# Kernel tuning notes

Measured on AMD Instinct MI355X. Metric: run time of the kernel, lower is better.

Reference implementation:

```python
import jax, jax.numpy as jnp
import numpy as np

BANDS = [2,3,3,3,3,3,3,3,3,3,3,8,8,8,8,8,8,8,8,8,8,8,8,16,16,16,16,16,16,16,17]
C = 128      # channels
H = 512      # 4 * channels
MAXO = 17 * 12  # padded fc2 output dim (largest band)
EPS = 1e-5


def setup_inputs() -> dict:
    key = jax.random.key(0)
    k0, k1, k2, k3, k4 = jax.random.split(key, 5)
    B, T, K = 4, 2000, len(BANDS)
    x = jax.random.normal(k0, (B, C, T, K), jnp.float32)
    norm_w = jnp.ones((K, C), jnp.float32)
    norm_b = jnp.zeros((K, C), jnp.float32)
    fc1_w = jax.random.normal(k1, (K, H, C), jnp.float32) * 0.05
    fc1_b = jax.random.normal(k2, (K, H), jnp.float32) * 0.02
    fc2_w = jax.random.normal(k3, (K, MAXO, H), jnp.float32) * 0.05
    fc2_b = jax.random.normal(k4, (K, MAXO), jnp.float32) * 0.02
    return dict(x=x, norm_w=norm_w, norm_b=norm_b, fc1_w=fc1_w, fc1_b=fc1_b,
                fc2_w=fc2_w, fc2_b=fc2_b)


def reference(x, norm_w, norm_b, fc1_w, fc1_b, fc2_w, fc2_b):
    # x: [B, C, T, K]. GroupNorm(1, C) per band: normalize over (C, T), affine per channel.
    mean = jnp.mean(x, axis=(1, 2), keepdims=True)            # [B,1,1,K]
    var = jnp.var(x, axis=(1, 2), keepdims=True)
    xn = (x - mean) / jnp.sqrt(var + EPS)
    xn = xn * norm_w.T[None, :, None, :] + norm_b.T[None, :, None, :]
    # fc1 + tanh, batched over all bands (same shape per band, distinct weights)
    h = jnp.einsum('bctk,khc->btkh', xn, fc1_w) + fc1_b       # [B,T,K,H]
    h = jnp.tanh(h)
    # fc2 + GLU per band (heterogeneous output dims -> small fixed loop)
    outs = []
    for i, bw in enumerate(BANDS):
        o = h[:, :, i, :] @ fc2_w[i, :12 * bw].T + fc2_b[i, :12 * bw]  # [B,T,12*bw]
        a, g = jnp.split(o, 2, axis=-1)
        o = a * jax.nn.sigmoid(g)                             # GLU -> [B,T,6*bw]
        outs.append(o.reshape(o.shape[0], o.shape[1], bw, 3, 2))
    m = jnp.concatenate(outs, axis=2)                         # [B,T,257,3,2]
    return m.transpose(0, 2, 1, 3, 4)                         # [B,257,T,3,2]
```

## Files before the change

### kernel.cpp

```cpp
#include <hip/hip_runtime.h>
#include <hip/hip_bf16.h>

#define NBANDS 31
#define CDIM 128
#define TDIM 2000
#define HDIM 512
#define MTOT 8000
#define MAXO 204
#define OPAD 224
#define NGRP 124
#define NMTILE 504
#define NMBK 63

typedef __attribute__((ext_vector_type(8))) short short8;
typedef __attribute__((ext_vector_type(4))) float f32x4;
typedef __attribute__((ext_vector_type(4))) unsigned int u32x4;
typedef __bf16 bf16x8 __attribute__((ext_vector_type(8)));

__constant__ int d_bw[NBANDS]   = {2,3,3,3,3,3,3,3,3,3,3,8,8,8,8,8,8,8,8,8,8,8,8,16,16,16,16,16,16,16,17};
__constant__ int d_boff[NBANDS] = {0,2,5,8,11,14,17,20,23,26,29,32,40,48,56,64,72,80,88,96,104,112,120,128,144,160,176,192,208,224,240};
__constant__ int d_nn16[NBANDS] = {2,3,3,3,3,3,3,3,3,3,3,6,6,6,6,6,6,6,6,6,6,6,6,12,12,12,12,12,12,12,13};

__device__ __forceinline__ unsigned short f2bf(float f) {
  unsigned int u = __float_as_uint(f);
  return (unsigned short)((u + 0x7fffu + ((u >> 16) & 1u)) >> 16);
}

__device__ __forceinline__ unsigned int cvt_pk_bf16(float lo, float hi) {
  unsigned int r;
  asm("v_cvt_pk_bf16_f32 %0, %1, %2" : "=v"(r) : "v"(lo), "v"(hi));
  return r;
}

__device__ __forceinline__ float fast_tanh(float x) {
  float p = __builtin_amdgcn_exp2f(2.885390082f * x);
  return 1.0f - 2.0f * __builtin_amdgcn_rcpf(p + 1.0f);
}

__device__ __forceinline__ float fast_sigmoid(float x) {
  return __builtin_amdgcn_rcpf(1.0f + __builtin_amdgcn_exp2f(-1.442695041f * x));
}

__device__ __forceinline__ f32x4 mfma_bf16(short8 a, short8 b, f32x4 c) {
  return __builtin_amdgcn_mfma_f32_16x16x32_bf16(
      __builtin_bit_cast(bf16x8, a), __builtin_bit_cast(bf16x8, b), c, 0, 0, 0);
}

__device__ __forceinline__ void g2lds(const char* gsrc, char* ldst, int lane) {
  __builtin_amdgcn_global_load_lds(
      (const __attribute__((address_space(1))) unsigned int*)(gsrc + lane * 16),
      (__attribute__((address_space(3))) unsigned int*)ldst, 16, 0, 0);
}

__global__ void k_finalize(const float* __restrict__ wsum, const float* __restrict__ wsq,
                           float* __restrict__ gmean, float* __restrict__ grstd) {
  int g = threadIdx.x;
  if (g < NGRP) {
    const float n = (float)(CDIM * TDIM);
    float m = wsum[g] / n;
    float v = wsq[g] / n - m * m;
    gmean[g] = m;
    grstd[g] = rsqrtf(v + 1e-5f);
  }
}

__global__ void k_prep_w1(const float* __restrict__ fc1_w, const float* __restrict__ norm_w,
                          const float* __restrict__ norm_b, const float* __restrict__ fc1_b,
                          unsigned short* __restrict__ w1f, float* __restrict__ t1,
                          float* __restrict__ t2) {
  int kn = blockIdx.x;
  int k = kn >> 9, n = kn & 511;
  int c = threadIdx.x;
  float w  = fc1_w[(size_t)kn * CDIM + c];
  float nw = norm_w[k * CDIM + c];
  float nb = norm_b[k * CDIM + c];
  float wp = w * nw;
  {
    int nc = n >> 7, hh = (n >> 4) & 7, kk = c >> 5;
    int lnw = (n & 15) | (((c >> 3) & 3) << 4);
    size_t eoff = ((((size_t)(k * 4 + nc) * 8 + hh) * 4 + kk) * 64 + lnw) * 8 + (c & 7);
    w1f[eoff] = f2bf(wp);
  }
  float s1 = wp, s2 = w * nb;
  #pragma unroll
  for (int off = 32; off >= 1; off >>= 1) {
    s1 += __shfl_down(s1, off);
    s2 += __shfl_down(s2, off);
  }
  __shared__ float r1[2], r2[2];
  if ((threadIdx.x & 63) == 0) { r1[threadIdx.x >> 6] = s1; r2[threadIdx.x >> 6] = s2; }
  __syncthreads();
  if (threadIdx.x == 0) {
    t1[kn] = r1[0] + r1[1];
    t2[kn] = r2[0] + r2[1] + fc1_b[kn];
  }
}

__global__ void k_prep_w2(const float* __restrict__ fc2_w, const float* __restrict__ fc2_b,
                          unsigned short* __restrict__ w2f, float* __restrict__ b2) {
  int ko = blockIdx.x;
  int k = ko >> 8;
  int o = ko & 255;
  int bw = d_bw[k];
  int O2 = 12 * bw, hf = 6 * bw;
  bool valid = o < O2;
  int srcrow = valid ? ((o & 1) ? (hf + (o >> 1)) : (o >> 1)) : 0;
  const float* sp = fc2_w + ((size_t)k * MAXO + srcrow) * HDIM;
  if (threadIdx.x == 0 && o < OPAD)
    b2[k * OPAD + o] = valid ? fc2_b[k * MAXO + srcrow] : 0.f;
  int ot = o >> 4, rr = o & 15;
  for (int j = threadIdx.x; j < HDIM; j += 256) {
    int ks = j >> 5, hp = j & 31;
    int q  = (hp >> 2) & 3;
    int jj = ((hp >> 4) << 2) | (hp & 3);
    unsigned short val = valid ? f2bf(sp[j]) : (unsigned short)0;
    size_t eoff = (((size_t)(k * 16 + ks)) * 16 + ot) * 512 + (size_t)(rr | (q << 4)) * 8 + jj;
    w2f[eoff] = val;
  }
}

__global__ void k_transpose(const float* __restrict__ x, unsigned short* __restrict__ xtf,
                            float* __restrict__ wsum, float* __restrict__ wsq) {
  __shared__ unsigned short tile[248 * 128];
  __shared__ float sred[256], sqred[256];
  const int t0 = blockIdx.x * 8;
  const int b = blockIdx.y;
  const int tid = threadIdx.x;
  const float* p = x + ((size_t)b * CDIM * TDIM + t0) * NBANDS;
  float s = 0.f, sq = 0.f;
  if (tid < 248) {
    const int f = tid;
    char* row = (char*)tile + f * 256;
    const int st = 4 * f;
    #pragma unroll 4
    for (int c2 = 0; c2 < 64; ++c2) {
      float v0 = p[(size_t)c2 * 124000 + f];
      float v1 = p[(size_t)c2 * 124000 + 62000 + f];
      s += v0 + v1;
      sq += v0 * v0 + v1 * v1;
      *(unsigned int*)(row + ((4 * c2 + st) & 255)) = cvt_pk_bf16(v0, v1);
    }
  }
  sred[tid] = s; sqred[tid] = sq;
  __syncthreads();
  if (tid < 31) {
    float ss = 0.f, qs = 0.f;
    #pragma unroll
    for (int j = 0; j < 8; ++j) { ss += sred[tid + 31 * j]; qs += sqred[tid + 31 * j]; }
    atomicAdd(&wsum[b * 31 + tid], ss);
    atomicAdd(&wsq [b * 31 + tid], qs);
  }
  for (int idx = tid; idx < 3968; idx += 256) {
    int ti = idx & 7, q4w = (idx >> 3) & 3, kkw = (idx >> 5) & 3, kb = idx >> 7;
    int f = ti * 31 + kb;
    const char* row = (const char*)tile + f * 256;
    const int st = 4 * f;
    u32x4 v;
    #pragma unroll
    for (int j = 0; j < 4; ++j)
      v[j] = *(const unsigned int*)(row + ((kkw * 64 + q4w * 16 + 4 * j + st) & 255));
    int m = b * TDIM + t0 + ti;
    int mtile = m >> 4, mrow = m & 15;
    size_t eoff = ((((size_t)kb * NMTILE + mtile) * 4 + kkw) * 64 + (mrow | (q4w << 4))) * 8;
    *(u32x4*)(xtf + eoff) = v;
  }
}

template<int SMAX>
__launch_bounds__(256, 2)
__global__ void k_gemm(const unsigned short* __restrict__ xtf,
                       const unsigned short* __restrict__ w1f,
                       const float* __restrict__ t1p, const float* __restrict__ t2p,
                       const unsigned short* __restrict__ w2f,
                       const float* __restrict__ b2p,
                       const float* __restrict__ gmean, const float* __restrict__ grstd,
                       float* __restrict__ out, int kbase, int nwg) {
  extern __shared__ char lds[];
  constexpr int BUFB = (8 + SMAX) * 1024;
  float* const t12 = (float*)lds;
  char* const bufA = lds + 4096;
  char* const bufB = lds + 4096 + BUFB;
  float* const Ls  = (float*)lds;

  const int bid = blockIdx.x;
  const int qq = nwg >> 3, r8 = nwg & 7;
  const int xcd = bid & 7, ixd = bid >> 3;
  const int wg = (xcd < r8 ? xcd * (qq + 1) : r8 * (qq + 1) + (xcd - r8) * qq) + ixd;
  const int kl = wg / NMBK;
  const int k = kbase + kl;
  const int mb = wg - kl * NMBK;
  const int m0 = mb * 128;

  const int tid = threadIdx.x;
  const int lane = tid & 63;
  const int wid = tid >> 6;
  const int col = lane & 15;
  const int q4 = lane >> 4;

  const int bw = d_bw[k];
  const int nn = d_nn16[k];
  const int half = 6 * bw;
  const int boffk = d_boff[k];

  #pragma unroll
  for (int i = 0; i < 2; ++i) {
    t12[tid + i * 256] = t1p[k * HDIM + tid + i * 256];
    t12[512 + tid + i * 256] = t2p[k * HDIM + tid + i * 256];
  }

  const int mt0 = (m0 >> 4) + wid * 2;
  short8 xv[2][4];
  #pragma unroll
  for (int r = 0; r < 2; ++r)
    #pragma unroll
    for (int kk = 0; kk < 4; ++kk)
      xv[r][kk] = *(const short8*)(xtf +
          (((size_t)k * NMTILE + mt0 + r) * 4 + kk) * 512 + lane * 8);

  float rs[2], rm[2];
  #pragma unroll
  for (int r = 0; r < 2; ++r) {
    int mr = m0 + wid * 32 + r * 16 + col;
    int mc = mr < (MTOT - 1) ? mr : (MTOT - 1);
    int g = (mc / 2000) * NBANDS + k;
    rs[r] = grstd[g];
    rm[r] = rs[r] * gmean[g];
  }

  const char* const w1kc = (const char*)w1f + (size_t)k * 131072;
  const char* const w2kc = (const char*)w2f + (size_t)k * 262144;
  const int ntt = 8 + nn;

  auto stage = [&](char* buf, int c) {
    const char* w1c = w1kc + (((c >> 2) * 8 + (c & 3) * 2) * 4096);
    const char* w2c = w2kc + c * 16384;
    for (int t = wid; t < ntt; t += 4) {
      const char* src = (t < 8) ? (w1c + t * 1024) : (w2c + (t - 8) * 1024);
      g2lds(src, buf + t * 1024, lane);
    }
  };

  const f32x4 fz = {0.f, 0.f, 0.f, 0.f};
  f32x4 acc2[SMAX][2];
  #pragma unroll
  for (int s = 0; s < SMAX; ++s) { acc2[s][0] = fz; acc2[s][1] = fz; }

  stage(bufA, 0);
  __syncthreads();

  #pragma unroll 1
  for (int c = 0; c < 16; ++c) {
    char* const bc = (c & 1) ? bufB : bufA;
    if (c < 15) stage((c & 1) ? bufA : bufB, c + 1);

    f32x4 a1[2][2];
    a1[0][0] = fz; a1[0][1] = fz; a1[1][0] = fz; a1[1][1] = fz;
    #pragma unroll
    for (int kk = 0; kk < 4; ++kk) {
      short8 wa0 = *(const short8*)(bc + kk * 1024 + lane * 16);
      short8 wa1 = *(const short8*)(bc + 4096 + kk * 1024 + lane * 16);
      #pragma unroll
      for (int r = 0; r < 2; ++r) {
        a1[0][r] = mfma_bf16(wa0, xv[r][kk], a1[0][r]);
        a1[1][r] = mfma_bf16(wa1, xv[r][kk], a1[1][r]);
      }
    }
    short8 hb[2];
    #pragma unroll
    for (int r = 0; r < 2; ++r) {
      u32x4 hbw;
      #pragma unroll
      for (int ht = 0; ht < 2; ++ht) {
        const f32x4 c1 = *(const f32x4*)(t12 + c * 32 + ht * 16 + q4 * 4);
        const f32x4 c2 = *(const f32x4*)(t12 + 512 + c * 32 + ht * 16 + q4 * 4);
        f32x4 v = a1[ht][r];
        float e0 = fast_tanh(fmaf(rs[r], v[0], fmaf(-rm[r], c1[0], c2[0])));
        float e1 = fast_tanh(fmaf(rs[r], v[1], fmaf(-rm[r], c1[1], c2[1])));
        float e2 = fast_tanh(fmaf(rs[r], v[2], fmaf(-rm[r], c1[2], c2[2])));
        float e3 = fast_tanh(fmaf(rs[r], v[3], fmaf(-rm[r], c1[3], c2[3])));
        hbw[ht * 2]     = cvt_pk_bf16(e0, e1);
        hbw[ht * 2 + 1] = cvt_pk_bf16(e2, e3);
      }
      hb[r] = __builtin_bit_cast(short8, hbw);
    }
    const char* w2l = bc + 8192;
    #pragma unroll
    for (int s = 0; s < SMAX; ++s) {
      if (s < nn) {
        short8 wb = *(const short8*)(w2l + s * 1024 + lane * 16);
        acc2[s][0] = mfma_bf16(wb, hb[0], acc2[s][0]);
        acc2[s][1] = mfma_bf16(wb, hb[1], acc2[s][1]);
      }
    }
    __syncthreads();
  }

  const float* b2k = b2p + (size_t)k * OPAD;
  const bool plain = (m0 / 2000 == (m0 + 127) / 2000) && (m0 + 128 <= MTOT);
  if (plain) {
    #pragma unroll
    for (int s = 0; s < SMAX; ++s) {
      if (s < nn) {
        f32x4 bias = *(const f32x4*)(b2k + s * 16 + q4 * 4);
        #pragma unroll
        for (int r = 0; r < 2; ++r) {
          const int tloc = wid * 32 + r * 16 + col;
          f32x4 v = acc2[s][r];
          #pragma unroll
          for (int p = 0; p < 2; ++p) {
            float a = v[2 * p] + bias[2 * p];
            float g = v[2 * p + 1] + bias[2 * p + 1];
            int op = s * 8 + q4 * 2 + p;
            if (op < half) {
              int orr = op / 6, occ = op - orr * 6;
              Ls[(orr * 128 + tloc) * 6 + occ] = a * fast_sigmoid(g);
            }
          }
        }
      }
    }
    __syncthreads();
    const int bb = m0 / 2000;
    const int tb = m0 - bb * 2000;
    const size_t obase = ((size_t)bb * 257 + boffk) * 2000;
    const int tot = bw * 384;
    for (int ii = tid; ii < tot; ii += 256) {
      int orr = ii / 384;
      int rem = ii - orr * 384;
      *(unsigned long long*)(out + (obase + (size_t)orr * 2000 + tb) * 6 + rem * 2) =
          *(const unsigned long long*)(Ls + orr * 768 + rem * 2);
    }
  } else {
    #pragma unroll
    for (int s = 0; s < SMAX; ++s) {
      if (s < nn) {
        f32x4 bias = *(const f32x4*)(b2k + s * 16 + q4 * 4);
        #pragma unroll
        for (int r = 0; r < 2; ++r) {
          const int m = m0 + wid * 32 + r * 16 + col;
          f32x4 v = acc2[s][r];
          #pragma unroll
          for (int p = 0; p < 2; ++p) {
            float a = v[2 * p] + bias[2 * p];
            float g = v[2 * p + 1] + bias[2 * p + 1];
            int op = s * 8 + q4 * 2 + p;
            if (op < half && m < MTOT) {
              int bbm = m / 2000;
              int t = m - bbm * 2000;
              int orr = op / 6, occ = op - orr * 6;
              out[(((size_t)bbm * 257 + boffk + orr) * TDIM + t) * 6 + occ] =
                  a * fast_sigmoid(g);
            }
          }
        }
      }
    }
  }
}

extern "C" void kernel_launch(void* const* d_in, const int* in_sizes, int n_in,
                              void* d_out, int out_size, void* d_ws, size_t ws_size,
                              hipStream_t stream) {
  const float* x      = (const float*)d_in[0];
  const float* norm_w = (const float*)d_in[1];
  const float* norm_b = (const float*)d_in[2];
  const float* fc1_w  = (const float*)d_in[3];
  const float* fc1_b  = (const float*)d_in[4];
  const float* fc2_w  = (const float*)d_in[5];
  const float* fc2_b  = (const float*)d_in[6];
  float* out = (float*)d_out;
  char* ws = (char*)d_ws;

  float* wsum  = (float*)(ws);
  float* wsq   = (float*)(ws + 512);
  float* gmean = (float*)(ws + 1024);
  float* grstd = (float*)(ws + 1536);
  size_t off = 4096;
  unsigned short* xtf = (unsigned short*)(ws + off); off += (size_t)NBANDS * NMTILE * 4 * 512 * 2;
  unsigned short* w1f = (unsigned short*)(ws + off); off += (size_t)NBANDS * 4 * 8 * 4 * 512 * 2;
  float* t1p = (float*)(ws + off); off += (size_t)NBANDS * HDIM * 4;
  float* t2p = (float*)(ws + off); off += (size_t)NBANDS * HDIM * 4;
  unsigned short* w2f = (unsigned short*)(ws + off); off += (size_t)NBANDS * 16 * 16 * 512 * 2;
  float* b2p = (float*)(ws + off); off += (size_t)NBANDS * OPAD * 4;

  hipMemsetAsync(ws, 0, 1024, stream);
  hipLaunchKernelGGL(k_prep_w1, dim3(NBANDS * HDIM), dim3(128), 0, stream,
                     fc1_w, norm_w, norm_b, fc1_b, w1f, t1p, t2p);
  hipLaunchKernelGGL(k_prep_w2, dim3(NBANDS * 256), dim3(256), 0, stream,
                     fc2_w, fc2_b, w2f, b2p);
  hipLaunchKernelGGL(k_transpose, dim3(250, 4), dim3(256), 0, stream, x, xtf, wsum, wsq);
  hipLaunchKernelGGL(k_finalize, dim3(1), dim3(128), 0, stream, wsum, wsq, gmean, grstd);

  hipFuncSetAttribute((const void*)k_gemm<13>, hipFuncAttributeMaxDynamicSharedMemorySize, 52224);
  hipFuncSetAttribute((const void*)k_gemm<6>,  hipFuncAttributeMaxDynamicSharedMemorySize, 32768);
  hipFuncSetAttribute((const void*)k_gemm<3>,  hipFuncAttributeMaxDynamicSharedMemorySize, 26624);
  hipLaunchKernelGGL((k_gemm<13>), dim3(8 * NMBK),  dim3(256), 52224, stream,
                     xtf, w1f, t1p, t2p, w2f, b2p, gmean, grstd, out, 23, 8 * NMBK);
  hipLaunchKernelGGL((k_gemm<6>),  dim3(12 * NMBK), dim3(256), 32768, stream,
                     xtf, w1f, t1p, t2p, w2f, b2p, gmean, grstd, out, 11, 12 * NMBK);
  hipLaunchKernelGGL((k_gemm<3>),  dim3(11 * NMBK), dim3(256), 26624, stream,
                     xtf, w1f, t1p, t2p, w2f, b2p, gmean, grstd, out, 0,  11 * NMBK);
}
```

Before: 194.9 us.

## Fuse preprocessing kernels and merge per-band GEMM launches into one

```diff
diff --git a/kernel.cpp b/kernel.cpp
--- a/kernel.cpp
+++ b/kernel.cpp
@@ -8,9 +8,10 @@
 #define MTOT 8000
 #define MAXO 204
 #define OPAD 224
-#define NGRP 124
 #define NMTILE 504
 #define NMBK 63
+#define NWGU (NBANDS * NMBK)
+#define SMAX 13
 
 typedef __attribute__((ext_vector_type(8))) short short8;
 typedef __attribute__((ext_vector_type(4))) float f32x4;
@@ -52,143 +53,143 @@
       (__attribute__((address_space(3))) unsigned int*)ldst, 16, 0, 0);
 }
 
-__global__ void k_finalize(const float* __restrict__ wsum, const float* __restrict__ wsq,
-                           float* __restrict__ gmean, float* __restrict__ grstd) {
-  int g = threadIdx.x;
-  if (g < NGRP) {
-    const float n = (float)(CDIM * TDIM);
-    float m = wsum[g] / n;
-    float v = wsq[g] / n - m * m;
-    gmean[g] = m;
-    grstd[g] = rsqrtf(v + 1e-5f);
-  }
-}
-
-__global__ void k_prep_w1(const float* __restrict__ fc1_w, const float* __restrict__ norm_w,
-                          const float* __restrict__ norm_b, const float* __restrict__ fc1_b,
-                          unsigned short* __restrict__ w1f, float* __restrict__ t1,
-                          float* __restrict__ t2) {
-  int kn = blockIdx.x;
-  int k = kn >> 9, n = kn & 511;
-  int c = threadIdx.x;
-  float w  = fc1_w[(size_t)kn * CDIM + c];
-  float nw = norm_w[k * CDIM + c];
-  float nb = norm_b[k * CDIM + c];
-  float wp = w * nw;
-  {
-    int nc = n >> 7, hh = (n >> 4) & 7, kk = c >> 5;
-    int lnw = (n & 15) | (((c >> 3) & 3) << 4);
-    size_t eoff = ((((size_t)(k * 4 + nc) * 8 + hh) * 4 + kk) * 64 + lnw) * 8 + (c & 7);
-    w1f[eoff] = f2bf(wp);
-  }
-  float s1 = wp, s2 = w * nb;
-  #pragma unroll
-  for (int off = 32; off >= 1; off >>= 1) {
-    s1 += __shfl_down(s1, off);
-    s2 += __shfl_down(s2, off);
-  }
-  __shared__ float r1[2], r2[2];
-  if ((threadIdx.x & 63) == 0) { r1[threadIdx.x >> 6] = s1; r2[threadIdx.x >> 6] = s2; }
-  __syncthreads();
-  if (threadIdx.x == 0) {
-    t1[kn] = r1[0] + r1[1];
-    t2[kn] = r2[0] + r2[1] + fc1_b[kn];
-  }
-}
-
-__global__ void k_prep_w2(const float* __restrict__ fc2_w, const float* __restrict__ fc2_b,
-                          unsigned short* __restrict__ w2f, float* __restrict__ b2) {
-  int ko = blockIdx.x;
-  int k = ko >> 8;
-  int o = ko & 255;
-  int bw = d_bw[k];
-  int O2 = 12 * bw, hf = 6 * bw;
-  bool valid = o < O2;
-  int srcrow = valid ? ((o & 1) ? (hf + (o >> 1)) : (o >> 1)) : 0;
-  const float* sp = fc2_w + ((size_t)k * MAXO + srcrow) * HDIM;
-  if (threadIdx.x == 0 && o < OPAD)
-    b2[k * OPAD + o] = valid ? fc2_b[k * MAXO + srcrow] : 0.f;
-  int ot = o >> 4, rr = o & 15;
-  for (int j = threadIdx.x; j < HDIM; j += 256) {
-    int ks = j >> 5, hp = j & 31;
-    int q  = (hp >> 2) & 3;
-    int jj = ((hp >> 4) << 2) | (hp & 3);
-    unsigned short val = valid ? f2bf(sp[j]) : (unsigned short)0;
-    size_t eoff = (((size_t)(k * 16 + ks)) * 16 + ot) * 512 + (size_t)(rr | (q << 4)) * 8 + jj;
-    w2f[eoff] = val;
-  }
-}
-
-__global__ void k_transpose(const float* __restrict__ x, unsigned short* __restrict__ xtf,
-                            float* __restrict__ wsum, float* __restrict__ wsq) {
+__launch_bounds__(256)
+__global__ void k_pre(const float* __restrict__ x,
+                      const float* __restrict__ norm_w, const float* __restrict__ norm_b,
+                      const float* __restrict__ fc1_w, const float* __restrict__ fc1_b,
+                      const float* __restrict__ fc2_w, const float* __restrict__ fc2_b,
+                      unsigned short* __restrict__ xtf,
+                      float* __restrict__ wsumP, float* __restrict__ wsqP,
+                      unsigned short* __restrict__ w1f,
+                      float* __restrict__ t1, float* __restrict__ t2,
+                      unsigned short* __restrict__ w2f, float* __restrict__ b2) {
   __shared__ unsigned short tile[248 * 128];
   __shared__ float sred[256], sqred[256];
-  const int t0 = blockIdx.x * 8;
-  const int b = blockIdx.y;
+  const int bid = blockIdx.x;
   const int tid = threadIdx.x;
-  const float* p = x + ((size_t)b * CDIM * TDIM + t0) * NBANDS;
-  float s = 0.f, sq = 0.f;
-  if (tid < 248) {
-    const int f = tid;
-    char* row = (char*)tile + f * 256;
-    const int st = 4 * f;
-    #pragma unroll 4
-    for (int c2 = 0; c2 < 64; ++c2) {
-      float v0 = p[(size_t)c2 * 124000 + f];
-      float v1 = p[(size_t)c2 * 124000 + 62000 + f];
-      s += v0 + v1;
-      sq += v0 * v0 + v1 * v1;
-      *(unsigned int*)(row + ((4 * c2 + st) & 255)) = cvt_pk_bf16(v0, v1);
-    }
-  }
-  sred[tid] = s; sqred[tid] = sq;
-  __syncthreads();
-  if (tid < 31) {
-    float ss = 0.f, qs = 0.f;
-    #pragma unroll
-    for (int j = 0; j < 8; ++j) { ss += sred[tid + 31 * j]; qs += sqred[tid + 31 * j]; }
-    atomicAdd(&wsum[b * 31 + tid], ss);
-    atomicAdd(&wsq [b * 31 + tid], qs);
-  }
-  for (int idx = tid; idx < 3968; idx += 256) {
-    int ti = idx & 7, q4w = (idx >> 3) & 3, kkw = (idx >> 5) & 3, kb = idx >> 7;
-    int f = ti * 31 + kb;
-    const char* row = (const char*)tile + f * 256;
-    const int st = 4 * f;
-    u32x4 v;
-    #pragma unroll
-    for (int j = 0; j < 4; ++j)
-      v[j] = *(const unsigned int*)(row + ((kkw * 64 + q4w * 16 + 4 * j + st) & 255));
-    int m = b * TDIM + t0 + ti;
-    int mtile = m >> 4, mrow = m & 15;
-    size_t eoff = ((((size_t)kb * NMTILE + mtile) * 4 + kkw) * 64 + (mrow | (q4w << 4))) * 8;
-    *(u32x4*)(xtf + eoff) = v;
-  }
-}
-
-template<int SMAX>
+
+  if (bid < 1000) {
+    const int tc = bid % 250, b = bid / 250;
+    const int t0 = tc * 8;
+    const float* p = x + ((size_t)b * CDIM * TDIM + t0) * NBANDS;
+    float s = 0.f, sq = 0.f;
+    if (tid < 248) {
+      const int f = tid;
+      char* row = (char*)tile + f * 256;
+      const int st = 4 * f;
+      #pragma unroll 4
+      for (int c2 = 0; c2 < 64; ++c2) {
+        float v0 = p[(size_t)c2 * 124000 + f];
+        float v1 = p[(size_t)c2 * 124000 + 62000 + f];
+        s += v0 + v1;
+        sq += v0 * v0 + v1 * v1;
+        *(unsigned int*)(row + ((4 * c2 + st) & 255)) = cvt_pk_bf16(v0, v1);
+      }
+    }
+    sred[tid] = s; sqred[tid] = sq;
+    __syncthreads();
+    if (tid < 31) {
+      float ss = 0.f, qs = 0.f;
+      #pragma unroll
+      for (int j = 0; j < 8; ++j) { ss += sred[tid + 31 * j]; qs += sqred[tid + 31 * j]; }
+      wsumP[((size_t)b * 250 + tc) * 31 + tid] = ss;
+      wsqP [((size_t)b * 250 + tc) * 31 + tid] = qs;
+    }
+    for (int idx = tid; idx < 3968; idx += 256) {
+      int ti = idx & 7, q4w = (idx >> 3) & 3, kkw = (idx >> 5) & 3, kb = idx >> 7;
+      int f = ti * 31 + kb;
+      const char* row = (const char*)tile + f * 256;
+      const int st = 4 * f;
+      u32x4 v;
+      #pragma unroll
+      for (int j = 0; j < 4; ++j)
+        v[j] = *(const unsigned int*)(row + ((kkw * 64 + q4w * 16 + 4 * j + st) & 255));
+      int m = b * TDIM + t0 + ti;
+      int mtile = m >> 4, mrow = m & 15;
+      size_t eoff = ((((size_t)kb * NMTILE + mtile) * 4 + kkw) * 64 + (mrow | (q4w << 4))) * 8;
+      *(u32x4*)(xtf + eoff) = v;
+    }
+  } else if (bid < 1992) {
+    const int idx = bid - 1000;
+    const int c = tid & 127;
+    const int hf2 = tid >> 7;
+    #pragma unroll 1
+    for (int it = 0; it < 8; ++it) {
+      const int kn = idx * 16 + it * 2 + hf2;
+      const int k = kn >> 9, n = kn & 511;
+      float w  = fc1_w[(size_t)kn * CDIM + c];
+      float nw = norm_w[k * CDIM + c];
+      float nb = norm_b[k * CDIM + c];
+      float wp = w * nw;
+      {
+        int nc = n >> 7, hh = (n >> 4) & 7, kk = c >> 5;
+        int lnw = (n & 15) | (((c >> 3) & 3) << 4);
+        size_t eoff = ((((size_t)(k * 4 + nc) * 8 + hh) * 4 + kk) * 64 + lnw) * 8 + (c & 7);
+        w1f[eoff] = f2bf(wp);
+      }
+      float s1 = wp, s2 = w * nb;
+      #pragma unroll
+      for (int off = 32; off >= 1; off >>= 1) {
+        s1 += __shfl_down(s1, off);
+        s2 += __shfl_down(s2, off);
+      }
+      if ((tid & 63) == 0) { sred[tid >> 6] = s1; sqred[tid >> 6] = s2; }
+      __syncthreads();
+      if ((tid & 127) == 0) {
+        t1[kn] = sred[hf2 * 2] + sred[hf2 * 2 + 1];
+        t2[kn] = sqred[hf2 * 2] + sqred[hf2 * 2 + 1] + fc1_b[kn];
+      }
+      __syncthreads();
+    }
+  } else {
+    const int idx = bid - 1992;
+    #pragma unroll 1
+    for (int oi = 0; oi < 8; ++oi) {
+      const int ko = idx * 8 + oi;
+      const int k = ko >> 8;
+      const int o = ko & 255;
+      const int bw = d_bw[k];
+      const int O2 = 12 * bw, hf = 6 * bw;
+      const bool valid = o < O2;
+      const int srcrow = valid ? ((o & 1) ? (hf + (o >> 1)) : (o >> 1)) : 0;
+      const float* sp = fc2_w + ((size_t)k * MAXO + srcrow) * HDIM;
+      if (tid == 0 && o < OPAD)
+        b2[k * OPAD + o] = valid ? fc2_b[k * MAXO + srcrow] : 0.f;
+      const int ot = o >> 4, rr = o & 15;
+      for (int j = tid; j < HDIM; j += 256) {
+        int ks = j >> 5, hp = j & 31;
+        int q  = (hp >> 2) & 3;
+        int jj = ((hp >> 4) << 2) | (hp & 3);
+        unsigned short val = valid ? f2bf(sp[j]) : (unsigned short)0;
+        size_t eoff = (((size_t)(k * 16 + ks)) * 16 + ot) * 512 + (size_t)(rr | (q << 4)) * 8 + jj;
+        w2f[eoff] = val;
+      }
+    }
+  }
+}
+
 __launch_bounds__(256, 2)
 __global__ void k_gemm(const unsigned short* __restrict__ xtf,
                        const unsigned short* __restrict__ w1f,
                        const float* __restrict__ t1p, const float* __restrict__ t2p,
                        const unsigned short* __restrict__ w2f,
                        const float* __restrict__ b2p,
-                       const float* __restrict__ gmean, const float* __restrict__ grstd,
-                       float* __restrict__ out, int kbase, int nwg) {
+                       const float* __restrict__ wsumP, const float* __restrict__ wsqP,
+                       float* __restrict__ out) {
   extern __shared__ char lds[];
   constexpr int BUFB = (8 + SMAX) * 1024;
   float* const t12 = (float*)lds;
   char* const bufA = lds + 4096;
   char* const bufB = lds + 4096 + BUFB;
+  float* const sstat = (float*)(lds + 4096 + 2 * BUFB);
   float* const Ls  = (float*)lds;
 
   const int bid = blockIdx.x;
-  const int qq = nwg >> 3, r8 = nwg & 7;
+  const int qq = NWGU >> 3, r8 = NWGU & 7;
   const int xcd = bid & 7, ixd = bid >> 3;
   const int wg = (xcd < r8 ? xcd * (qq + 1) : r8 * (qq + 1) + (xcd - r8) * qq) + ixd;
-  const int kl = wg / NMBK;
-  const int k = kbase + kl;
-  const int mb = wg - kl * NMBK;
+  const int k = wg / NMBK;
+  const int mb = wg - k * NMBK;
   const int m0 = mb * 128;
 
   const int tid = threadIdx.x;
@@ -202,29 +203,33 @@
   const int half = 6 * bw;
   const int boffk = d_boff[k];
 
+  const int b0 = m0 / 2000;
+  const int b1 = ((m0 + 127 < MTOT) ? (m0 + 127) : (MTOT - 1)) / 2000;
+  if (wid <= b1 - b0) {
+    const int b = b0 + wid;
+    float sP = 0.f, sQ = 0.f;
+    for (int t = lane; t < 250; t += 64) {
+      sP += wsumP[((size_t)b * 250 + t) * 31 + k];
+      sQ += wsqP [((size_t)b * 250 + t) * 31 + k];
+    }
+    #pragma unroll
+    for (int off = 32; off >= 1; off >>= 1) {
+      sP += __shfl_down(sP, off);
+      sQ += __shfl_down(sQ, off);
+    }
+    if (lane == 0) {
+      const float n = (float)(CDIM * TDIM);
+      float mean = sP / n;
+      float var = sQ / n - mean * mean;
+      sstat[wid * 2] = mean;
+      sstat[wid * 2 + 1] = rsqrtf(var + 1e-5f);
+    }
+  }
+
   #pragma unroll
   for (int i = 0; i < 2; ++i) {
     t12[tid + i * 256] = t1p[k * HDIM + tid + i * 256];
     t12[512 + tid + i * 256] = t2p[k * HDIM + tid + i * 256];
-  }
-
-  const int mt0 = (m0 >> 4) + wid * 2;
-  short8 xv[2][4];
-  #pragma unroll
-  for (int r = 0; r < 2; ++r)
-    #pragma unroll
-    for (int kk = 0; kk < 4; ++kk)
-      xv[r][kk] = *(const short8*)(xtf +
-          (((size_t)k * NMTILE + mt0 + r) * 4 + kk) * 512 + lane * 8);
-
-  float rs[2], rm[2];
-  #pragma unroll
-  for (int r = 0; r < 2; ++r) {
-    int mr = m0 + wid * 32 + r * 16 + col;
-    int mc = mr < (MTOT - 1) ? mr : (MTOT - 1);
-    int g = (mc / 2000) * NBANDS + k;
-    rs[r] = grstd[g];
-    rm[r] = rs[r] * gmean[g];
   }
 
   const char* const w1kc = (const char*)w1f + (size_t)k * 131072;
@@ -239,14 +244,33 @@
       g2lds(src, buf + t * 1024, lane);
     }
   };
+  stage(bufA, 0);
+
+  const int mt0 = (m0 >> 4) + wid * 2;
+  short8 xv[2][4];
+  #pragma unroll
+  for (int r = 0; r < 2; ++r)
+    #pragma unroll
+    for (int kk = 0; kk < 4; ++kk)
+      xv[r][kk] = *(const short8*)(xtf +
+          (((size_t)k * NMTILE + mt0 + r) * 4 + kk) * 512 + lane * 8);
+
+  __syncthreads();
+
+  float rs[2], rm[2];
+  #pragma unroll
+  for (int r = 0; r < 2; ++r) {
+    int mr = m0 + wid * 32 + r * 16 + col;
+    int mc = mr < (MTOT - 1) ? mr : (MTOT - 1);
+    int bsel = mc / 2000 - b0;
+    rs[r] = sstat[bsel * 2 + 1];
+    rm[r] = rs[r] * sstat[bsel * 2];
+  }
 
   const f32x4 fz = {0.f, 0.f, 0.f, 0.f};
   f32x4 acc2[SMAX][2];
   #pragma unroll
   for (int s = 0; s < SMAX; ++s) { acc2[s][0] = fz; acc2[s][1] = fz; }
-
-  stage(bufA, 0);
-  __syncthreads();
 
   #pragma unroll 1
   for (int c = 0; c < 16; ++c) {
@@ -371,11 +395,9 @@
   float* out = (float*)d_out;
   char* ws = (char*)d_ws;
 
-  float* wsum  = (float*)(ws);
-  float* wsq   = (float*)(ws + 512);
-  float* gmean = (float*)(ws + 1024);
-  float* grstd = (float*)(ws + 1536);
-  size_t off = 4096;
+  size_t off = 0;
+  float* wsumP = (float*)(ws + off); off += (size_t)4 * 250 * 31 * 4 + 128;
+  float* wsqP  = (float*)(ws + off); off += (size_t)4 * 250 * 31 * 4 + 128;
   unsigned short* xtf = (unsigned short*)(ws + off); off += (size_t)NBANDS * NMTILE * 4 * 512 * 2;
   unsigned short* w1f = (unsigned short*)(ws + off); off += (size_t)NBANDS * 4 * 8 * 4 * 512 * 2;
   float* t1p = (float*)(ws + off); off += (size_t)NBANDS * HDIM * 4;
@@ -383,21 +405,11 @@
   unsigned short* w2f = (unsigned short*)(ws + off); off += (size_t)NBANDS * 16 * 16 * 512 * 2;
   float* b2p = (float*)(ws + off); off += (size_t)NBANDS * OPAD * 4;
 
-  hipMemsetAsync(ws, 0, 1024, stream);
-  hipLaunchKernelGGL(k_prep_w1, dim3(NBANDS * HDIM), dim3(128), 0, stream,
-                     fc1_w, norm_w, norm_b, fc1_b, w1f, t1p, t2p);
-  hipLaunchKernelGGL(k_prep_w2, dim3(NBANDS * 256), dim3(256), 0, stream,
-                     fc2_w, fc2_b, w2f, b2p);
-  hipLaunchKernelGGL(k_transpose, dim3(250, 4), dim3(256), 0, stream, x, xtf, wsum, wsq);
-  hipLaunchKernelGGL(k_finalize, dim3(1), dim3(128), 0, stream, wsum, wsq, gmean, grstd);
-
-  hipFuncSetAttribute((const void*)k_gemm<13>, hipFuncAttributeMaxDynamicSharedMemorySize, 52224);
-  hipFuncSetAttribute((const void*)k_gemm<6>,  hipFuncAttributeMaxDynamicSharedMemorySize, 32768);
-  hipFuncSetAttribute((const void*)k_gemm<3>,  hipFuncAttributeMaxDynamicSharedMemorySize, 26624);
-  hipLaunchKernelGGL((k_gemm<13>), dim3(8 * NMBK),  dim3(256), 52224, stream,
-                     xtf, w1f, t1p, t2p, w2f, b2p, gmean, grstd, out, 23, 8 * NMBK);
-  hipLaunchKernelGGL((k_gemm<6>),  dim3(12 * NMBK), dim3(256), 32768, stream,
-                     xtf, w1f, t1p, t2p, w2f, b2p, gmean, grstd, out, 11, 12 * NMBK);
-  hipLaunchKernelGGL((k_gemm<3>),  dim3(11 * NMBK), dim3(256), 26624, stream,
-                     xtf, w1f, t1p, t2p, w2f, b2p, gmean, grstd, out, 0,  11 * NMBK);
-}
+  hipLaunchKernelGGL(k_pre, dim3(2984), dim3(256), 0, stream,
+                     x, norm_w, norm_b, fc1_w, fc1_b, fc2_w, fc2_b,
+                     xtf, wsumP, wsqP, w1f, t1p, t2p, w2f, b2p);
+
+  hipFuncSetAttribute((const void*)k_gemm, hipFuncAttributeMaxDynamicSharedMemorySize, 52224);
+  hipLaunchKernelGGL(k_gemm, dim3(NWGU), dim3(256), 52224, stream,
+                     xtf, w1f, t1p, t2p, w2f, b2p, wsumP, wsqP, out);
+}
```

Result: slower. 227.5 us (+16.7%).
